# Kernel optimization log

Hardware: AMD Instinct MI355X
Metric: run time of the kernel (lower is better)

Reference implementation:

```python
import jax, jax.numpy as jnp
from jax import lax
import numpy as np

T = 3          # num_frame
DIV = 2        # channel_shift div
PAD = 1        # kernel_size//2 (same padding for k=3)


def setup_inputs() -> dict:
    key = jax.random.key(0)
    k1, k2 = jax.random.split(key)
    x = jax.random.normal(k1, (12, 64, 256, 256), dtype=jnp.float32)      # (B*T, C, H, W)
    weight = jax.random.normal(k2, (64, 64, 3, 3), dtype=jnp.float32)     # (O, I, kh, kw)
    return {"x": x, "weight": weight}


def reference(x, weight):
    BT, C, H, W = x.shape
    B = BT // T
    # channel_shift: view (B, T*C, H, W), roll by C//div along channel axis
    shift = C // DIV
    y = x.reshape(B, T * C, H, W)
    y = jnp.roll(y, shift, axis=1).reshape(BT, C, H, W)
    # BinaryConv2d: sign(activations), sign(weights) * per-out-channel mean|W|
    scale = jnp.mean(jnp.abs(weight), axis=(1, 2, 3), keepdims=True)      # (O,1,1,1)
    bw = jnp.sign(weight) * scale
    bx = jnp.sign(y)
    out = lax.conv_general_dilated(
        bx, bw,
        window_strides=(1, 1),
        padding=[(PAD, PAD), (PAD, PAD)],
        dimension_numbers=("NCHW", "OIHW", "NCHW"),
    )
    return out
```

## Files before the change

### kernel.cpp

```cpp
#include <hip/hip_runtime.h>
#include <stdint.h>

typedef unsigned long long u64;
typedef unsigned int u32;
typedef int i32x4 __attribute__((ext_vector_type(4)));

#define HW 65536
#define WD 256
#define ROWB (258 * 64)
#define RS (258 * ROWB)

__global__ __launch_bounds__(64) void pack_w2(const float* __restrict__ wt,
                                              char* __restrict__ sw,
                                              float* __restrict__ scale) {
    const int o = blockIdx.x;
    const int c = threadIdx.x;
    const float* p = wt + o * 576 + c * 9;
    float s = 0.f;
#pragma unroll
    for (int k = 0; k < 9; k++) {
        const u32 u = __float_as_uint(p[k]);
        s += fabsf(p[k]);
        sw[k * 4096 + o * 64 + c] = (char)(1 + (((int)u >> 31) & 0xFE));
    }
#pragma unroll
    for (int off = 32; off > 0; off >>= 1) s += __shfl_down(s, off);
    if (c == 0) scale[o] = s * (1.0f / 576.0f);
}

__global__ __launch_bounds__(320) void zero_tb(char* __restrict__ sx) {
    const int n = blockIdx.x >> 1;
    const int row = (blockIdx.x & 1) * 257;
    const int t = threadIdx.x;
    if (t < 258) {
        uint4 z = make_uint4(0, 0, 0, 0);
        uint4* d = (uint4*)(sx + (size_t)n * RS + (size_t)row * ROWB + t * 64);
        d[0] = z; d[1] = z; d[2] = z; d[3] = z;
    }
}

__global__ __launch_bounds__(256) void pack_x2(const float* __restrict__ x,
                                               char* __restrict__ sx) {
    const int band = blockIdx.x;
    const int n = blockIdx.y;
    const int wv = threadIdx.x >> 6;
    const int lane = threadIdx.x & 63;
    const int r = (band << 2) + wv;

    const int b = n / 3;
    const int t = n - b * 3;
    const int fp = b * 3 + (t + 2) % 3;

    const float* xa = x + ((size_t)fp * 64 + 32) * HW + r * WD + (lane << 2);
    const float* xb = x + (size_t)n * 64 * HW + r * WD + (lane << 2);

    char* dstrow = sx + (size_t)n * RS + (size_t)(r + 1) * ROWB;

#pragma unroll
    for (int cc = 0; cc < 4; cc++) {
        const float* base = (cc < 2) ? (xa + (size_t)(cc * 16) * HW)
                                     : (xb + (size_t)((cc - 2) * 16) * HW);
        u32 w0[4] = {0, 0, 0, 0}, w1[4] = {0, 0, 0, 0};
        u32 w2[4] = {0, 0, 0, 0}, w3[4] = {0, 0, 0, 0};
#pragma unroll
        for (int ci = 0; ci < 16; ci++) {
            float4 v = *(const float4*)(base + (size_t)ci * HW);
            const int sh = (ci & 3) * 8;
            const int wi = ci >> 2;
            w0[wi] |= (1u + ((u32)((int)__float_as_uint(v.x) >> 31) & 0xFEu)) << sh;
            w1[wi] |= (1u + ((u32)((int)__float_as_uint(v.y) >> 31) & 0xFEu)) << sh;
            w2[wi] |= (1u + ((u32)((int)__float_as_uint(v.z) >> 31) & 0xFEu)) << sh;
            w3[wi] |= (1u + ((u32)((int)__float_as_uint(v.w) >> 31) & 0xFEu)) << sh;
        }
        char* d = dstrow + (size_t)((lane << 2) + 1) * 64 + cc * 16;
        *(uint4*)(d)       = make_uint4(w0[0], w0[1], w0[2], w0[3]);
        *(uint4*)(d + 64)  = make_uint4(w1[0], w1[1], w1[2], w1[3]);
        *(uint4*)(d + 128) = make_uint4(w2[0], w2[1], w2[2], w2[3]);
        *(uint4*)(d + 192) = make_uint4(w3[0], w3[1], w3[2], w3[3]);
    }

    if (threadIdx.x < 8) {
        const int rr = (band << 2) + (threadIdx.x >> 1) + 1;
        const int col = (threadIdx.x & 1) * 257;
        uint4 z = make_uint4(0, 0, 0, 0);
        uint4* d = (uint4*)(sx + (size_t)n * RS + (size_t)rr * ROWB + (size_t)col * 64);
        d[0] = z; d[1] = z; d[2] = z; d[3] = z;
    }
}

__global__ __launch_bounds__(256, 2) void conv_mfma(const char* __restrict__ sx,
                                                    const char* __restrict__ sw,
                                                    const float* __restrict__ scale,
                                                    float* __restrict__ out) {
    const int bx = blockIdx.x;
    const int n = blockIdx.y;
    const int gh = ((bx & 7) << 5) | (bx >> 3);
    const int lane = threadIdx.x & 63;
    const int wv = threadIdx.x >> 6;
    const int lr = lane & 15;
    const int q = lane >> 4;

    i32x4 a[4][9];
#pragma unroll
    for (int og = 0; og < 4; og++)
#pragma unroll
        for (int tap = 0; tap < 9; tap++)
            a[og][tap] = *(const i32x4*)(sw + (size_t)(tap * 64 + og * 16 + lr) * 64 + q * 16);

    float sc[4][4];
#pragma unroll
    for (int og = 0; og < 4; og++)
#pragma unroll
        for (int reg = 0; reg < 4; reg++)
            sc[og][reg] = scale[og * 16 + q * 4 + reg];

    const char* sxn = sx + (size_t)n * RS;
    float* ob = out + (size_t)n * 64 * HW + gh * WD;
    const int px0w = wv << 6;

#pragma unroll
    for (int pxg = 0; pxg < 4; pxg++) {
        const int px0 = px0w + (pxg << 4);
        i32x4 bfr[9];
#pragma unroll
        for (int tr = 0; tr < 3; tr++)
#pragma unroll
            for (int tc = 0; tc < 3; tc++)
                bfr[tr * 3 + tc] = *(const i32x4*)(sxn
                    + (size_t)(gh + tr) * ROWB
                    + (size_t)(px0 + lr + tc) * 64 + q * 16);

#pragma unroll
        for (int og = 0; og < 4; og++) {
            i32x4 acc = {0, 0, 0, 0};
#pragma unroll
            for (int tap = 0; tap < 9; tap++)
                acc = __builtin_amdgcn_mfma_i32_16x16x64_i8(a[og][tap], bfr[tap], acc, 0, 0, 0);
#pragma unroll
            for (int reg = 0; reg < 4; reg++) {
                const int o = og * 16 + q * 4 + reg;
                ob[(size_t)o * HW + px0 + lr] = sc[og][reg] * (float)acc[reg];
            }
        }
    }
}

extern "C" void kernel_launch(void* const* d_in, const int* in_sizes, int n_in,
                              void* d_out, int out_size, void* d_ws, size_t ws_size,
                              hipStream_t stream) {
    (void)in_sizes; (void)n_in; (void)out_size; (void)ws_size;
    const float* x  = (const float*)d_in[0];
    const float* wt = (const float*)d_in[1];
    float* out = (float*)d_out;

    char* sx = (char*)d_ws;
    char* sw = sx + (size_t)12 * RS;
    float* scale = (float*)(sw + 9 * 4096);

    pack_w2<<<64, 64, 0, stream>>>(wt, sw, scale);
    zero_tb<<<24, 320, 0, stream>>>(sx);
    pack_x2<<<dim3(64, 12), 256, 0, stream>>>(x, sx);
    conv_mfma<<<dim3(256, 12), 256, 0, stream>>>(sx, sw, scale, out);
}
```

Baseline: 434.7 us.

## Fuse sign-packing of activations into conv kernel via LDS row staging

Removes the global int8 packed-activation buffer and its zero/pack kernels. Each block now loads four input rows (two output rows plus halo) straight from the fp32 input, sign-packs them into swizzled LDS, and runs the int8 MFMA conv from LDS, handling column padding with masks. The goal is to cut the global write and re-read of the packed tensor and two kernel launches. In exchange each input row is loaded and packed twice, once per adjacent band, and each wave now holds only half the output-channel weight fragments.

Measured after the change: 357.3 us. 1.22x faster.

```diff
diff --git a/kernel.cpp b/kernel.cpp
--- a/kernel.cpp
+++ b/kernel.cpp
@@ -7,8 +7,7 @@
 
 #define HW 65536
 #define WD 256
-#define ROWB (258 * 64)
-#define RS (258 * ROWB)
+#define LROWB 16384
 
 __global__ __launch_bounds__(64) void pack_w2(const float* __restrict__ wt,
                                               char* __restrict__ sw,
@@ -28,119 +27,122 @@
     if (c == 0) scale[o] = s * (1.0f / 576.0f);
 }
 
-__global__ __launch_bounds__(320) void zero_tb(char* __restrict__ sx) {
-    const int n = blockIdx.x >> 1;
-    const int row = (blockIdx.x & 1) * 257;
-    const int t = threadIdx.x;
-    if (t < 258) {
-        uint4 z = make_uint4(0, 0, 0, 0);
-        uint4* d = (uint4*)(sx + (size_t)n * RS + (size_t)row * ROWB + t * 64);
-        d[0] = z; d[1] = z; d[2] = z; d[3] = z;
-    }
-}
+__global__ __launch_bounds__(512, 4) void fused_mfma(const float* __restrict__ x,
+                                                     const char* __restrict__ sw,
+                                                     const float* __restrict__ scale,
+                                                     float* __restrict__ out) {
+    __shared__ __align__(16) char lds[4 * LROWB];
 
-__global__ __launch_bounds__(256) void pack_x2(const float* __restrict__ x,
-                                               char* __restrict__ sx) {
-    const int band = blockIdx.x;
-    const int n = blockIdx.y;
-    const int wv = threadIdx.x >> 6;
-    const int lane = threadIdx.x & 63;
-    const int r = (band << 2) + wv;
+    const int bx = blockIdx.x;
+    const int n  = blockIdx.y;
+    const int band = ((bx & 7) << 4) | (bx >> 3);
+    const int gh0 = band << 1;
 
     const int b = n / 3;
     const int t = n - b * 3;
     const int fp = b * 3 + (t + 2) % 3;
 
-    const float* xa = x + ((size_t)fp * 64 + 32) * HW + r * WD + (lane << 2);
-    const float* xb = x + (size_t)n * 64 * HW + r * WD + (lane << 2);
+    const int tid  = threadIdx.x;
+    const int lane = tid & 63;
+    const int wv   = tid >> 6;
+    const int q    = lane >> 4;
+    const int lr   = lane & 15;
 
-    char* dstrow = sx + (size_t)n * RS + (size_t)(r + 1) * ROWB;
+    {
+        const int r  = wv >> 1;
+        const int s  = wv & 1;
+        const int ir = gh0 - 1 + r;
 
+        u32 st[4][8];
 #pragma unroll
-    for (int cc = 0; cc < 4; cc++) {
-        const float* base = (cc < 2) ? (xa + (size_t)(cc * 16) * HW)
-                                     : (xb + (size_t)((cc - 2) * 16) * HW);
-        u32 w0[4] = {0, 0, 0, 0}, w1[4] = {0, 0, 0, 0};
-        u32 w2[4] = {0, 0, 0, 0}, w3[4] = {0, 0, 0, 0};
+        for (int j = 0; j < 4; j++)
 #pragma unroll
-        for (int ci = 0; ci < 16; ci++) {
-            float4 v = *(const float4*)(base + (size_t)ci * HW);
-            const int sh = (ci & 3) * 8;
-            const int wi = ci >> 2;
-            w0[wi] |= (1u + ((u32)((int)__float_as_uint(v.x) >> 31) & 0xFEu)) << sh;
-            w1[wi] |= (1u + ((u32)((int)__float_as_uint(v.y) >> 31) & 0xFEu)) << sh;
-            w2[wi] |= (1u + ((u32)((int)__float_as_uint(v.z) >> 31) & 0xFEu)) << sh;
-            w3[wi] |= (1u + ((u32)((int)__float_as_uint(v.w) >> 31) & 0xFEu)) << sh;
+            for (int k = 0; k < 8; k++) st[j][k] = 0;
+
+        if ((ir >= 0) & (ir < 256)) {
+            const float* src = s ? (x + (size_t)n * 64 * HW)
+                                 : (x + ((size_t)fp * 64 + 32) * HW);
+            const float* p = src + (size_t)ir * WD + (lane << 2);
+#pragma unroll
+            for (int c = 0; c < 32; c++) {
+                float4 v = *(const float4*)(p + (size_t)c * HW);
+                const int wi = c >> 2;
+                const int sh = (c & 3) * 8;
+                st[0][wi] |= (1u + (((u32)((int)__float_as_uint(v.x) >> 31)) & 0xFEu)) << sh;
+                st[1][wi] |= (1u + (((u32)((int)__float_as_uint(v.y) >> 31)) & 0xFEu)) << sh;
+                st[2][wi] |= (1u + (((u32)((int)__float_as_uint(v.z) >> 31)) & 0xFEu)) << sh;
+                st[3][wi] |= (1u + (((u32)((int)__float_as_uint(v.w) >> 31)) & 0xFEu)) << sh;
+            }
         }
-        char* d = dstrow + (size_t)((lane << 2) + 1) * 64 + cc * 16;
-        *(uint4*)(d)       = make_uint4(w0[0], w0[1], w0[2], w0[3]);
-        *(uint4*)(d + 64)  = make_uint4(w1[0], w1[1], w1[2], w1[3]);
-        *(uint4*)(d + 128) = make_uint4(w2[0], w2[1], w2[2], w2[3]);
-        *(uint4*)(d + 192) = make_uint4(w3[0], w3[1], w3[2], w3[3]);
+        const int sw2 = lane & 3;
+#pragma unroll
+        for (int j = 0; j < 4; j++) {
+            char* dbase = lds + r * LROWB + (((lane << 2) + j) << 6);
+#pragma unroll
+            for (int tt = 0; tt < 2; tt++) {
+                const int swz = ((s << 1) + tt) ^ sw2;
+                i32x4 val = {(int)st[j][tt * 4 + 0], (int)st[j][tt * 4 + 1],
+                             (int)st[j][tt * 4 + 2], (int)st[j][tt * 4 + 3]};
+                *(i32x4*)(dbase + (swz << 4)) = val;
+            }
+        }
     }
 
-    if (threadIdx.x < 8) {
-        const int rr = (band << 2) + (threadIdx.x >> 1) + 1;
-        const int col = (threadIdx.x & 1) * 257;
-        uint4 z = make_uint4(0, 0, 0, 0);
-        uint4* d = (uint4*)(sx + (size_t)n * RS + (size_t)rr * ROWB + (size_t)col * 64);
-        d[0] = z; d[1] = z; d[2] = z; d[3] = z;
-    }
-}
-
-__global__ __launch_bounds__(256, 2) void conv_mfma(const char* __restrict__ sx,
-                                                    const char* __restrict__ sw,
-                                                    const float* __restrict__ scale,
-                                                    float* __restrict__ out) {
-    const int bx = blockIdx.x;
-    const int n = blockIdx.y;
-    const int gh = ((bx & 7) << 5) | (bx >> 3);
-    const int lane = threadIdx.x & 63;
-    const int wv = threadIdx.x >> 6;
-    const int lr = lane & 15;
-    const int q = lane >> 4;
-
-    i32x4 a[4][9];
+    const int pq = wv & 3;
+    const int oh = wv >> 2;
+    i32x4 a[2][9];
 #pragma unroll
-    for (int og = 0; og < 4; og++)
+    for (int j = 0; j < 2; j++) {
+        const int og = oh * 2 + j;
 #pragma unroll
         for (int tap = 0; tap < 9; tap++)
-            a[og][tap] = *(const i32x4*)(sw + (size_t)(tap * 64 + og * 16 + lr) * 64 + q * 16);
+            a[j][tap] = *(const i32x4*)(sw + (size_t)(tap * 4096 + (og * 16 + lr) * 64 + (q << 4)));
+    }
+    float4 s4[2];
+#pragma unroll
+    for (int j = 0; j < 2; j++)
+        s4[j] = *(const float4*)(scale + (oh << 5) + (j << 4) + (q << 2));
 
-    float sc[4][4];
+    __syncthreads();
+
+    const int rl = pq >> 1;
+    const int colbase = (pq & 1) << 7;
+    const int gh = gh0 + rl;
+    float* ob = out + (size_t)n * 64 * HW + (size_t)gh * WD;
+
+#pragma unroll 1
+    for (int pxg = 0; pxg < 8; pxg++) {
+        const int cc0 = colbase + (pxg << 4);
+        const int c = cc0 + lr;
+        const int cm  = (c == 0)   ? 0   : c - 1;
+        const int cp2 = (c == 255) ? 255 : c + 1;
+        const bool zl = (c == 0);
+        const bool zr = (c == 255);
+
+        i32x4 acc0 = {0, 0, 0, 0}, acc1 = {0, 0, 0, 0};
 #pragma unroll
-    for (int og = 0; og < 4; og++)
+        for (int tr = 0; tr < 3; tr++) {
+            const char* rb = lds + (rl + tr) * LROWB;
+            i32x4 f0 = *(const i32x4*)(rb + (cm  << 6) + (((q ^ ((cm  >> 2) & 3))) << 4));
+            i32x4 f1 = *(const i32x4*)(rb + (c   << 6) + (((q ^ ((c   >> 2) & 3))) << 4));
+            i32x4 f2 = *(const i32x4*)(rb + (cp2 << 6) + (((q ^ ((cp2 >> 2) & 3))) << 4));
+            if (zl) f0 = (i32x4){0, 0, 0, 0};
+            if (zr) f2 = (i32x4){0, 0, 0, 0};
+            acc0 = __builtin_amdgcn_mfma_i32_16x16x64_i8(a[0][tr * 3 + 0], f0, acc0, 0, 0, 0);
+            acc1 = __builtin_amdgcn_mfma_i32_16x16x64_i8(a[1][tr * 3 + 0], f0, acc1, 0, 0, 0);
+            acc0 = __builtin_amdgcn_mfma_i32_16x16x64_i8(a[0][tr * 3 + 1], f1, acc0, 0, 0, 0);
+            acc1 = __builtin_amdgcn_mfma_i32_16x16x64_i8(a[1][tr * 3 + 1], f1, acc1, 0, 0, 0);
+            acc0 = __builtin_amdgcn_mfma_i32_16x16x64_i8(a[0][tr * 3 + 2], f2, acc0, 0, 0, 0);
+            acc1 = __builtin_amdgcn_mfma_i32_16x16x64_i8(a[1][tr * 3 + 2], f2, acc1, 0, 0, 0);
+        }
+
+        const float* sc0 = (const float*)&s4[0];
+        const float* sc1 = (const float*)&s4[1];
 #pragma unroll
-        for (int reg = 0; reg < 4; reg++)
-            sc[og][reg] = scale[og * 16 + q * 4 + reg];
-
-    const char* sxn = sx + (size_t)n * RS;
-    float* ob = out + (size_t)n * 64 * HW + gh * WD;
-    const int px0w = wv << 6;
-
-#pragma unroll
-    for (int pxg = 0; pxg < 4; pxg++) {
-        const int px0 = px0w + (pxg << 4);
-        i32x4 bfr[9];
-#pragma unroll
-        for (int tr = 0; tr < 3; tr++)
-#pragma unroll
-            for (int tc = 0; tc < 3; tc++)
-                bfr[tr * 3 + tc] = *(const i32x4*)(sxn
-                    + (size_t)(gh + tr) * ROWB
-                    + (size_t)(px0 + lr + tc) * 64 + q * 16);
-
-#pragma unroll
-        for (int og = 0; og < 4; og++) {
-            i32x4 acc = {0, 0, 0, 0};
-#pragma unroll
-            for (int tap = 0; tap < 9; tap++)
-                acc = __builtin_amdgcn_mfma_i32_16x16x64_i8(a[og][tap], bfr[tap], acc, 0, 0, 0);
-#pragma unroll
-            for (int reg = 0; reg < 4; reg++) {
-                const int o = og * 16 + q * 4 + reg;
-                ob[(size_t)o * HW + px0 + lr] = sc[og][reg] * (float)acc[reg];
-            }
+        for (int reg = 0; reg < 4; reg++) {
+            const int o0 = (oh << 5) + (q << 2) + reg;
+            ob[(size_t)o0 * HW + c]        = sc0[reg] * (float)acc0[reg];
+            ob[(size_t)(o0 + 16) * HW + c] = sc1[reg] * (float)acc1[reg];
         }
     }
 }
@@ -153,12 +155,9 @@
     const float* wt = (const float*)d_in[1];
     float* out = (float*)d_out;
 
-    char* sx = (char*)d_ws;
-    char* sw = sx + (size_t)12 * RS;
+    char* sw = (char*)d_ws;
     float* scale = (float*)(sw + 9 * 4096);
 
     pack_w2<<<64, 64, 0, stream>>>(wt, sw, scale);
-    zero_tb<<<24, 320, 0, stream>>>(sx);
-    pack_x2<<<dim3(64, 12), 256, 0, stream>>>(x, sx);
-    conv_mfma<<<dim3(256, 12), 256, 0, stream>>>(sx, sw, scale, out);
+    fused_mfma<<<dim3(128, 12), 512, 0, stream>>>(x, sw, scale, out);
 }
```
